# Performance work log

Measured on AMD Instinct MI355X. Metric: run time of the kernel, lower is better.

The kernel has to match this reference:

```python
import jax, jax.numpy as jnp
import numpy as np

B, S, HID = 1, 1024, 4096
H, D = 32, 128
KB, NUM_SLOTS, KB_IDX = 2048, 2, 0
TOPK = 100
THETA = 10000.0
KB_SCALE = 100.0
NEG = -1e9


def _rope(x, pos):
    # x: [B,H,S,D], pos: [B,S]
    inv = 1.0 / (THETA ** (jnp.arange(0, D, 2, dtype=jnp.float32) / D))
    freqs = pos[..., None].astype(jnp.float32) * inv          # [B,S,D/2]
    emb = jnp.concatenate([freqs, freqs], -1)                  # [B,S,D]
    cos = jnp.cos(emb)[:, None]                                # [B,1,S,D]
    sin = jnp.sin(emb)[:, None]
    x1, x2 = jnp.split(x, 2, -1)
    rot = jnp.concatenate([-x2, x1], -1)
    return x * cos + rot * sin


def setup_inputs() -> dict:
    key = jax.random.key(0)
    ks = jax.random.split(key, 8)
    hidden_states = jax.random.normal(ks[0], (B, S, HID), jnp.float32)
    # standard additive causal mask (0 on allowed, large negative above diagonal)
    causal = jnp.tril(jnp.ones((S, S), bool))
    attention_mask = jnp.where(causal, 0.0, NEG).astype(jnp.float32)[None, None]
    position_ids = jnp.arange(S, dtype=jnp.int64 if jax.config.jax_enable_x64 else jnp.int32)[None].astype(jnp.int32)
    kb_keys = jax.random.normal(ks[1], (KB, NUM_SLOTS * HID), jnp.float32)
    kb_values = jax.random.normal(ks[2], (KB, NUM_SLOTS * HID), jnp.float32)
    std = 0.02
    Wq = jax.random.normal(ks[3], (HID, HID), jnp.float32) * std
    Wq2 = jax.random.normal(ks[4], (HID, HID), jnp.float32) * std
    Wk = jax.random.normal(ks[5], (HID, HID), jnp.float32) * std
    Wv = jax.random.normal(ks[6], (HID, HID), jnp.float32) * std
    Wo = jax.random.normal(ks[7], (HID, HID), jnp.float32) * std
    score_shift = jnp.zeros((H, 1), jnp.float32) - 3.0
    return dict(hidden_states=hidden_states, attention_mask=attention_mask,
                position_ids=position_ids, kb_keys=kb_keys, kb_values=kb_values,
                Wq=Wq, Wq2=Wq2, Wk=Wk, Wv=Wv, Wo=Wo, score_shift=score_shift)


def reference(hidden_states, attention_mask, position_ids, kb_keys, kb_values,
              Wq, Wq2, Wk, Wv, Wo, score_shift):
    b, s, _ = hidden_states.shape
    heads = lambda x: x.reshape(b, s, H, D).transpose(0, 2, 1, 3)
    q = heads(hidden_states @ Wq.T)
    q2 = heads(hidden_states @ Wq2.T)
    k = heads(hidden_states @ Wk.T)
    v = heads(hidden_states @ Wv.T)
    q = _rope(q, position_ids)
    k = _rope(k, position_ids)
    scale = 1.0 / jnp.sqrt(jnp.asarray(D, jnp.float32))

    # ---- KB branch (2-dim kb_kvs, layer_idx % kb_layer_frequency == 0) ----
    kbk = kb_keys.reshape(KB, NUM_SLOTS, HID)[:, KB_IDX].reshape(KB, H, D).transpose(1, 0, 2)  # [H,KB,D]
    kbv = kb_values.reshape(KB, NUM_SLOTS, HID)[:, KB_IDX].reshape(KB, H, D).transpose(1, 0, 2)
    kbk = jnp.broadcast_to(kbk[None], (b, H, KB, D))
    kbv = jnp.broadcast_to(kbv[None], (b, H, KB, D))

    # dynamic_sparsify: top-k pruning of KB entries by summed q2-scores
    aw2_full = jnp.einsum('bhqd,bhkd->bhqk', q2, kbk) * scale     # [b,H,S,KB]
    kb_scores = jax.lax.stop_gradient(aw2_full.sum((1, 2)))       # [b,KB]
    _, top_idx = jax.lax.top_k(kb_scores, TOPK)                   # [b,TOPK]
    gather = jax.vmap(lambda a, i: a[:, i])                        # [H,KB,D],[TOPK]->[H,TOPK,D]
    kbk_t = gather(kbk, top_idx)
    kbv_t = gather(kbv, top_idx)

    keys = jnp.concatenate([kbk_t, k], 2)                         # [b,H,TOPK+S,D]
    vals = jnp.concatenate([kbv_t, v], 2)

    aw = jnp.einsum('bhqd,bhkd->bhqk', q, keys) * scale           # [b,H,S,TOPK+S]

    # sep_query_head: KB logits use q2, per-head score_shift, log scale-factor correction
    aw2 = jnp.einsum('bhqd,bhkd->bhqk', q2, kbk_t) * scale        # [b,H,S,TOPK]
    aw2 = aw2 + score_shift.reshape(1, H, 1, 1)
    aw2 = aw2 - jnp.log(jnp.asarray(TOPK, jnp.float32)) + jnp.log(jnp.asarray(KB_SCALE, jnp.float32))
    aw = jnp.concatenate([aw2, aw[..., TOPK:]], -1)

    # mask: KB columns fully visible (no fully-padded rows in causal mask)
    kb_mask = jnp.zeros((b, 1, s, TOPK), attention_mask.dtype)
    mask = jnp.concatenate([kb_mask, attention_mask], -1)
    probs = jax.nn.softmax((aw + mask).astype(jnp.float32), -1).astype(q.dtype)

    out = jnp.einsum('bhqk,bhkd->bhqd', probs, vals)
    out = out.transpose(0, 2, 1, 3).reshape(b, s, HID)
    return out @ Wo.T
```

## Files before the change

### kernel.cpp

```cpp
#include <hip/hip_runtime.h>
#include <hip/hip_bf16.h>
#include <math.h>

typedef __hip_bfloat16 bf16_t;
typedef __attribute__((ext_vector_type(8))) short short8;
typedef __attribute__((ext_vector_type(4))) float f32x4;

#define S_LEN 1024
#define HID   4096
#define NH    32
#define HD    128
#define KB_N  2048
#define TOPK  100
#define SCALE 0.08838834764831845f

typedef const __attribute__((address_space(1))) void* gptr_t;
typedef __attribute__((address_space(3))) void* lptr_t;

__global__ void k0_zero(float* __restrict__ out, float* __restrict__ hssum) {
  int tid = threadIdx.x;
  if (blockIdx.x < 4096) {
    float4 z = {0.f, 0.f, 0.f, 0.f};
    *(float4*)(out + ((size_t)blockIdx.x * 256 + tid) * 4) = z;
  } else {
    float4 z = {0.f, 0.f, 0.f, 0.f};
    *(float4*)(hssum + tid * 4) = z;
    *(float4*)(hssum + 1024 + tid * 4) = z;
    *(float4*)(hssum + 2048 + tid * 4) = z;
    *(float4*)(hssum + 3072 + tid * 4) = z;
  }
}

__global__ void kw_conv(const float* __restrict__ Wq, const float* __restrict__ Wq2,
                        const float* __restrict__ Wk, const float* __restrict__ Wv,
                        const float* __restrict__ Wo,
                        bf16_t* __restrict__ Wcat, bf16_t* __restrict__ Wob) {
  int w = blockIdx.y;
  const float* src = (w == 0) ? Wq : (w == 1) ? Wq2 : (w == 2) ? Wk : (w == 3) ? Wv : Wo;
  bf16_t* dst = (w < 4) ? (Wcat + (size_t)w * 16777216) : Wob;
  size_t i = ((size_t)blockIdx.x * 256 + threadIdx.x) * 4;
  float4 f = *(const float4*)(src + i);
  union { bf16_t h[4]; uint2 u; } p;
  p.h[0] = __float2bfloat16(f.x); p.h[1] = __float2bfloat16(f.y);
  p.h[2] = __float2bfloat16(f.z); p.h[3] = __float2bfloat16(f.w);
  *(uint2*)(dst + i) = p.u;
}

__global__ void k1_convert(const float* __restrict__ hs, bf16_t* __restrict__ hsb) {
  size_t i = ((size_t)blockIdx.x * 256 + threadIdx.x) * 4;
  float4 f = *(const float4*)(hs + i);
  union { bf16_t h[4]; uint2 u; } p;
  p.h[0] = __float2bfloat16(f.x); p.h[1] = __float2bfloat16(f.y);
  p.h[2] = __float2bfloat16(f.z); p.h[3] = __float2bfloat16(f.w);
  *(uint2*)(hsb + i) = p.u;
}

__global__ void k1_colsum(const float* __restrict__ hs, float* __restrict__ hssum) {
  int col = blockIdx.x * 256 + threadIdx.x;
  int r0 = blockIdx.y * 64;
  float acc = 0.f;
#pragma unroll 8
  for (int r = 0; r < 64; r++) acc += hs[(size_t)(r0 + r) * HID + col];
  atomicAdd(hssum + col, acc);
}

__global__ void k2_q2sum(const float* __restrict__ W,
                         const float* __restrict__ hssum,
                         float* __restrict__ q2sum) {
  int wave = threadIdx.x >> 6, lane = threadIdx.x & 63;
  int row = blockIdx.x * 4 + wave;
  const float4* wr = (const float4*)(W + (size_t)row * HID);
  const float4* xr = (const float4*)hssum;
  float acc = 0.f;
#pragma unroll
  for (int it = 0; it < 16; it++) {
    float4 a = wr[it * 64 + lane];
    float4 b = xr[it * 64 + lane];
    acc += a.x * b.x + a.y * b.y + a.z * b.z + a.w * b.w;
  }
#pragma unroll
  for (int off = 32; off > 0; off >>= 1) acc += __shfl_xor(acc, off, 64);
  if (lane == 0) q2sum[row] = acc;
}

__global__ void k3_kbscore(const float* __restrict__ kbk,
                           const float* __restrict__ q2sum,
                           float* __restrict__ scores) {
  int wave = threadIdx.x >> 6, lane = threadIdx.x & 63;
  int row = blockIdx.x * 4 + wave;
  const float4* kr = (const float4*)(kbk + (size_t)row * 8192);
  const float4* xr = (const float4*)q2sum;
  float acc = 0.f;
#pragma unroll
  for (int it = 0; it < 16; it++) {
    float4 a = kr[it * 64 + lane];
    float4 b = xr[it * 64 + lane];
    acc += a.x * b.x + a.y * b.y + a.z * b.z + a.w * b.w;
  }
#pragma unroll
  for (int off = 32; off > 0; off >>= 1) acc += __shfl_xor(acc, off, 64);
  if (lane == 0) scores[row] = acc * SCALE;
}

__global__ void k4_topk(const float* __restrict__ scores, int* __restrict__ tidx) {
  int lane = threadIdx.x;
  float v[32];
#pragma unroll
  for (int i = 0; i < 32; i++) v[i] = scores[i * 64 + lane];
  for (int t = 0; t < TOPK; t++) {
    float bm = -INFINITY; int bi = 0x7fffffff;
#pragma unroll
    for (int i = 0; i < 32; i++) {
      if (v[i] > bm) { bm = v[i]; bi = i * 64 + lane; }
    }
#pragma unroll
    for (int off = 32; off > 0; off >>= 1) {
      float ov = __shfl_xor(bm, off, 64);
      int   oi = __shfl_xor(bi, off, 64);
      if (ov > bm || (ov == bm && oi < bi)) { bm = ov; bi = oi; }
    }
    if (lane == 0) tidx[t] = bi;
    if ((bi & 63) == lane) {
      int slot = bi >> 6;
#pragma unroll
      for (int i = 0; i < 32; i++) if (i == slot) v[i] = -INFINITY;
    }
  }
}

__global__ void k5_gather(const float* __restrict__ kbk, const float* __restrict__ kbv,
                          const int* __restrict__ tidx,
                          bf16_t* __restrict__ kbkt, bf16_t* __restrict__ kbvt) {
  int j = blockIdx.x;
  int tid = threadIdx.x;
  if (j < TOPK) {
    size_t src = (size_t)tidx[j] * 8192;
#pragma unroll
    for (int r = 0; r < 4; r++) {
      int i = (tid + r * 256) * 4;
      float4 a = *(const float4*)(kbk + src + i);
      float4 b = *(const float4*)(kbv + src + i);
      union { bf16_t h[4]; uint2 u; } pa, pb;
      pa.h[0] = __float2bfloat16(a.x); pa.h[1] = __float2bfloat16(a.y);
      pa.h[2] = __float2bfloat16(a.z); pa.h[3] = __float2bfloat16(a.w);
      pb.h[0] = __float2bfloat16(b.x); pb.h[1] = __float2bfloat16(b.y);
      pb.h[2] = __float2bfloat16(b.z); pb.h[3] = __float2bfloat16(b.w);
      *(uint2*)(kbkt + (size_t)j * HID + i) = pa.u;
      *(uint2*)(kbvt + (size_t)j * HID + i) = pb.u;
    }
  } else {
    uint2 z; z.x = 0u; z.y = 0u;
#pragma unroll
    for (int r = 0; r < 4; r++) {
      int i = (tid + r * 256) * 4;
      *(uint2*)(kbkt + (size_t)j * HID + i) = z;
      *(uint2*)(kbvt + (size_t)j * HID + i) = z;
    }
  }
}

template<int MODE>
__global__ __launch_bounds__(256) void gemm_dma(
    const bf16_t* __restrict__ A, const bf16_t* __restrict__ B,
    void* O0, void* O1, void* O2, void* O3) {
  __shared__ bf16_t As[128 * 32];
  __shared__ bf16_t Bs[128 * 32];
  const int tid = threadIdx.x;
  const int wave = tid >> 6, lane = tid & 63;
  const int bm = blockIdx.y * 128;
  const int bn = blockIdx.x * 128;
  const int lrow = lane & 15, quad = lane >> 4;
  const int wr = wave >> 1, wc = wave & 1;
  const int srow = lane >> 2, sch = lane & 3;

  f32x4 acc[4][4];
  const f32x4 zero4 = {0.f, 0.f, 0.f, 0.f};
#pragma unroll
  for (int i = 0; i < 4; i++)
#pragma unroll
    for (int j = 0; j < 4; j++) acc[i][j] = zero4;

  const int kbeg = (MODE == 1) ? blockIdx.z * 1024 : 0;
  const int kend = (MODE == 1) ? kbeg + 1024 : 4096;

  for (int k0 = kbeg; k0 < kend; k0 += 32) {
    __syncthreads();
#pragma unroll
    for (int h = 0; h < 2; h++) {
      int rg = wave * 32 + h * 16;
      __builtin_amdgcn_global_load_lds(
          (gptr_t)(A + (size_t)(bm + rg + srow) * 4096 + k0 + sch * 8),
          (lptr_t)(As + rg * 32), 16, 0, 0);
      __builtin_amdgcn_global_load_lds(
          (gptr_t)(B + (size_t)(bn + rg + srow) * 4096 + k0 + sch * 8),
          (lptr_t)(Bs + rg * 32), 16, 0, 0);
    }
    __syncthreads();
    short8 af[4], bfr[4];
#pragma unroll
    for (int i = 0; i < 4; i++)
      af[i] = *(const short8*)(As + (wr * 64 + i * 16 + lrow) * 32 + quad * 8);
#pragma unroll
    for (int j = 0; j < 4; j++)
      bfr[j] = *(const short8*)(Bs + (wc * 64 + j * 16 + lrow) * 32 + quad * 8);
#pragma unroll
    for (int i = 0; i < 4; i++)
#pragma unroll
      for (int j = 0; j < 4; j++)
        acc[i][j] = __builtin_amdgcn_mfma_f32_16x16x32_bf16(af[i], bfr[j], acc[i][j], 0, 0, 0);
  }

  if (MODE == 0) {
    bf16_t* dst = (bf16_t*)((bn >> 12) == 0 ? O0 : (bn >> 12) == 1 ? O1
                          : (bn >> 12) == 2 ? O2 : O3);
    int nb = bn & 4095;
#pragma unroll
    for (int i = 0; i < 4; i++)
#pragma unroll
      for (int j = 0; j < 4; j++)
#pragma unroll
        for (int r = 0; r < 4; r++) {
          int m = bm + wr * 64 + i * 16 + quad * 4 + r;
          int n = nb + wc * 64 + j * 16 + lrow;
          dst[(size_t)m * 4096 + n] = __float2bfloat16(acc[i][j][r]);
        }
  } else {
    float* dst = (float*)O0;
#pragma unroll
    for (int i = 0; i < 4; i++)
#pragma unroll
      for (int j = 0; j < 4; j++)
#pragma unroll
        for (int r = 0; r < 4; r++) {
          int m = bm + wr * 64 + i * 16 + quad * 4 + r;
          int n = bn + wc * 64 + j * 16 + lrow;
          atomicAdd(dst + (size_t)m * 4096 + n, acc[i][j][r]);
        }
  }
}

template<int OUT_BF16>
__global__ __launch_bounds__(256) void gemm_bt(
    const bf16_t* __restrict__ A,
    const float* __restrict__ B0, const float* __restrict__ B1,
    const float* __restrict__ B2, const float* __restrict__ B3,
    void* C0, void* C1, void* C2, void* C3) {
  const int z = blockIdx.z;
  const float* __restrict__ B = (z == 0) ? B0 : (z == 1) ? B1 : (z == 2) ? B2 : B3;
  void* Cv = (z == 0) ? C0 : (z == 1) ? C1 : (z == 2) ? C2 : C3;
  __shared__ bf16_t As[128][40];
  __shared__ bf16_t Bs[128][40];
  const int tid = threadIdx.x;
  const int bm = blockIdx.y * 128, bn = blockIdx.x * 128;
  const int wave = tid >> 6, lane = tid & 63;
  const int wr = wave >> 1, wc = wave & 1;
  const int lrow = lane & 15, quad = lane >> 4;
  f32x4 acc[4][4];
  const f32x4 zero4 = {0.f, 0.f, 0.f, 0.f};
#pragma unroll
  for (int i = 0; i < 4; i++)
#pragma unroll
    for (int j = 0; j < 4; j++) acc[i][j] = zero4;
  const int arow = tid >> 2, ach = tid & 3;
  const int brow = tid >> 3, bch = tid & 7;
  for (int k0 = 0; k0 < 4096; k0 += 32) {
    __syncthreads();
#pragma unroll
    for (int r = 0; r < 2; r++) {
      int row = arow + r * 64;
      uint4 val = *(const uint4*)(A + (size_t)(bm + row) * 4096 + k0 + ach * 8);
      *(uint4*)(&As[row][ach * 8]) = val;
    }
#pragma unroll
    for (int r = 0; r < 4; r++) {
      int row = brow + r * 32;
      float4 f = *(const float4*)(B + (size_t)(bn + row) * 4096 + k0 + bch * 4);
      union { bf16_t h[4]; uint2 u; } p;
      p.h[0] = __float2bfloat16(f.x); p.h[1] = __float2bfloat16(f.y);
      p.h[2] = __float2bfloat16(f.z); p.h[3] = __float2bfloat16(f.w);
      *(uint2*)(&Bs[row][bch * 4]) = p.u;
    }
    __syncthreads();
    short8 af[4], bfr[4];
#pragma unroll
    for (int i = 0; i < 4; i++)
      af[i] = *(const short8*)(&As[wr * 64 + i * 16 + lrow][quad * 8]);
#pragma unroll
    for (int j = 0; j < 4; j++)
      bfr[j] = *(const short8*)(&Bs[wc * 64 + j * 16 + lrow][quad * 8]);
#pragma unroll
    for (int i = 0; i < 4; i++)
#pragma unroll
      for (int j = 0; j < 4; j++)
        acc[i][j] = __builtin_amdgcn_mfma_f32_16x16x32_bf16(af[i], bfr[j], acc[i][j], 0, 0, 0);
  }
#pragma unroll
  for (int i = 0; i < 4; i++)
#pragma unroll
    for (int j = 0; j < 4; j++)
#pragma unroll
      for (int r = 0; r < 4; r++) {
        int m = bm + wr * 64 + i * 16 + quad * 4 + r;
        int n = bn + wc * 64 + j * 16 + lrow;
        if (OUT_BF16)
          ((bf16_t*)Cv)[(size_t)m * 4096 + n] = __float2bfloat16(acc[i][j][r]);
        else
          ((float*)Cv)[(size_t)m * 4096 + n] = acc[i][j][r];
      }
}

__global__ void k7_rope(bf16_t* __restrict__ q, bf16_t* __restrict__ k,
                        const int* __restrict__ pos_ids) {
  int t = blockIdx.x * 256 + threadIdx.x;
  int d = t & 63;
  int h = (t >> 6) & 31;
  int s = t >> 11;
  float pos = (float)pos_ids[s];
  float inv = exp2f(-(float)d * 0.20762050593046f);
  float ang = pos * inv;
  float c = cosf(ang), si = sinf(ang);
  size_t i1 = (size_t)s * HID + h * HD + d;
  size_t i2 = i1 + 64;
  float a1 = __bfloat162float(q[i1]), a2 = __bfloat162float(q[i2]);
  q[i1] = __float2bfloat16(a1 * c - a2 * si);
  q[i2] = __float2bfloat16(a2 * c + a1 * si);
  float b1 = __bfloat162float(k[i1]), b2 = __bfloat162float(k[i2]);
  k[i1] = __float2bfloat16(b1 * c - b2 * si);
  k[i2] = __float2bfloat16(b2 * c + b1 * si);
}

#define FA_PAD 136
__global__ __launch_bounds__(256) void k8_flash(
    const bf16_t* __restrict__ qg, const bf16_t* __restrict__ q2g,
    const bf16_t* __restrict__ kg, const bf16_t* __restrict__ vg,
    const bf16_t* __restrict__ kbkt, const bf16_t* __restrict__ kbvt,
    const float* __restrict__ shift_p,
    bf16_t* __restrict__ outb) {
  __shared__ bf16_t KV[128][FA_PAD];
  __shared__ bf16_t Ps[4][16][FA_PAD];
  int qt = 15 - (int)blockIdx.x;
  int h = blockIdx.y;
  int q0 = qt * 64;
  int tid = threadIdx.x;
  int wave = tid >> 6, lane = tid & 63;
  int lrow = lane & 15, quad = lane >> 4;

  short8 qf[4], q2f[4];
  {
    const size_t base = (size_t)(q0 + wave * 16 + lrow) * HID + h * HD;
#pragma unroll
    for (int kc = 0; kc < 4; kc++) {
      qf[kc]  = *(const short8*)(qg  + base + kc * 32 + quad * 8);
      q2f[kc] = *(const short8*)(q2g + base + kc * 32 + quad * 8);
    }
  }
  const f32x4 zero4 = {0.f, 0.f, 0.f, 0.f};
  f32x4 O[8];
#pragma unroll
  for (int df = 0; df < 8; df++) O[df] = zero4;
  float m_i[4], l_i[4];
#pragma unroll
  for (int r = 0; r < 4; r++) { m_i[r] = -INFINITY; l_i[r] = 0.f; }
  float shift = shift_p[h];

  int nt = (q0 + 63) / 128 + 1;
  for (int tile = -1; tile < nt; tile++) {
    const bf16_t* ksrc = (tile < 0) ? (kbkt + h * HD)
                                    : (kg + (size_t)tile * 128 * HID + h * HD);
    const bf16_t* vsrc = (tile < 0) ? (kbvt + h * HD)
                                    : (vg + (size_t)tile * 128 * HID + h * HD);
    __syncthreads();
    {
      int rbase = tid >> 4, ch = tid & 15;
#pragma unroll
      for (int rr = 0; rr < 8; rr++) {
        int row = rr * 16 + rbase;
        uint4 val = *(const uint4*)(ksrc + (size_t)row * HID + ch * 8);
        *(uint4*)(&KV[row][ch * 8]) = val;
      }
    }
    __syncthreads();
    f32x4 Sv[8];
#pragma unroll
    for (int jf = 0; jf < 8; jf++) {
      short8 kf[4];
#pragma unroll
      for (int kc = 0; kc < 4; kc++)
        kf[kc] = *(const short8*)(&KV[jf * 16 + lrow][kc * 32 + quad * 8]);
      f32x4 s = zero4;
      if (tile < 0) {
#pragma unroll
        for (int kc = 0; kc < 4; kc++)
          s = __builtin_amdgcn_mfma_f32_16x16x32_bf16(q2f[kc], kf[kc], s, 0, 0, 0);
      } else {
#pragma unroll
        for (int kc = 0; kc < 4; kc++)
          s = __builtin_amdgcn_mfma_f32_16x16x32_bf16(qf[kc], kf[kc], s, 0, 0, 0);
      }
      Sv[jf] = s;
    }
#pragma unroll
    for (int jf = 0; jf < 8; jf++)
#pragma unroll
      for (int r = 0; r < 4; r++) {
        float val = Sv[jf][r] * SCALE;
        if (tile < 0) {
          val += shift;
          int col = jf * 16 + lrow;
          if (col >= TOPK) val = -1e30f;
        } else {
          int srow = q0 + wave * 16 + quad * 4 + r;
          int tcol = tile * 128 + jf * 16 + lrow;
          if (tcol > srow) val -= 1e9f;
        }
        Sv[jf][r] = val;
      }
    float alpha[4];
#pragma unroll
    for (int r = 0; r < 4; r++) {
      float tm = Sv[0][r];
#pragma unroll
      for (int jf = 1; jf < 8; jf++) tm = fmaxf(tm, Sv[jf][r]);
#pragma unroll
      for (int off = 1; off < 16; off <<= 1) tm = fmaxf(tm, __shfl_xor(tm, off, 64));
      float mn = fmaxf(m_i[r], tm);
      alpha[r] = __expf(m_i[r] - mn);
      m_i[r] = mn;
    }
    float rsum[4] = {0.f, 0.f, 0.f, 0.f};
#pragma unroll
    for (int jf = 0; jf < 8; jf++)
#pragma unroll
      for (int r = 0; r < 4; r++) {
        float p = __expf(Sv[jf][r] - m_i[r]);
        Sv[jf][r] = p;
        rsum[r] += p;
      }
#pragma unroll
    for (int r = 0; r < 4; r++) {
#pragma unroll
      for (int off = 1; off < 16; off <<= 1) rsum[r] += __shfl_xor(rsum[r], off, 64);
      l_i[r] = l_i[r] * alpha[r] + rsum[r];
    }
#pragma unroll
    for (int jf = 0; jf < 8; jf++)
#pragma unroll
      for (int r = 0; r < 4; r++)
        Ps[wave][quad * 4 + r][jf * 16 + lrow] = __float2bfloat16(Sv[jf][r]);
#pragma unroll
    for (int df = 0; df < 8; df++)
#pragma unroll
      for (int r = 0; r < 4; r++) O[df][r] *= alpha[r];
    __syncthreads();
    {
      int rbase = tid >> 4, ch = tid & 15;
#pragma unroll
      for (int rr = 0; rr < 8; rr++) {
        int t = rr * 16 + rbase;
        union { uint4 u; bf16_t hx[8]; } vv;
        vv.u = *(const uint4*)(vsrc + (size_t)t * HID + ch * 8);
        int cs = ((t >> 3) ^ ch) & 15;
        int tl = t & 7;
#pragma unroll
        for (int e = 0; e < 8; e++)
          KV[ch * 8 + e][cs * 8 + tl] = vv.hx[e];
      }
    }
    __syncthreads();
    short8 pf[4];
#pragma unroll
    for (int kc = 0; kc < 4; kc++)
      pf[kc] = *(const short8*)(&Ps[wave][lrow][kc * 32 + quad * 8]);
#pragma unroll
    for (int df = 0; df < 8; df++) {
      int d = df * 16 + lrow;
      int sw = (d >> 3) & 15;
#pragma unroll
      for (int kc = 0; kc < 4; kc++) {
        short8 vf = *(const short8*)(&KV[d][(((kc * 4 + quad) ^ sw) & 15) * 8]);
        O[df] = __builtin_amdgcn_mfma_f32_16x16x32_bf16(pf[kc], vf, O[df], 0, 0, 0);
      }
    }
  }
#pragma unroll
  for (int df = 0; df < 8; df++)
#pragma unroll
    for (int r = 0; r < 4; r++) {
      int srow = q0 + wave * 16 + quad * 4 + r;
      float val = O[df][r] / l_i[r];
      outb[(size_t)srow * HID + h * HD + df * 16 + lrow] = __float2bfloat16(val);
    }
}

extern "C" void kernel_launch(void* const* d_in, const int* in_sizes, int n_in,
                              void* d_out, int out_size, void* d_ws, size_t ws_size,
                              hipStream_t stream) {
  const float* hs    = (const float*)d_in[0];
  const int*   pos   = (const int*)d_in[2];
  const float* kbk   = (const float*)d_in[3];
  const float* kbv   = (const float*)d_in[4];
  const float* Wq    = (const float*)d_in[5];
  const float* Wq2   = (const float*)d_in[6];
  const float* Wk    = (const float*)d_in[7];
  const float* Wv    = (const float*)d_in[8];
  const float* Wo    = (const float*)d_in[9];
  const float* shift = (const float*)d_in[10];
  float* out = (float*)d_out;

  char* ws = (char*)d_ws;
  const size_t MB8 = 8388608;
  bf16_t* qb    = (bf16_t*)(ws);
  bf16_t* q2b   = (bf16_t*)(ws + MB8);
  bf16_t* kbuf  = (bf16_t*)(ws + 2 * MB8);
  bf16_t* vbuf  = (bf16_t*)(ws + 3 * MB8);
  bf16_t* hsb   = (bf16_t*)(ws + 4 * MB8);
  bf16_t* kbkt  = (bf16_t*)(ws + 5 * MB8);
  bf16_t* kbvt  = (bf16_t*)(ws + 5 * MB8 + 1048576);
  float*  hssum = (float*)(ws + 5 * MB8 + 2 * 1048576);
  float*  q2s   = (float*)(ws + 5 * MB8 + 2 * 1048576 + 16384);
  float*  scr   = (float*)(ws + 5 * MB8 + 2 * 1048576 + 32768);
  int*    tidx  = (int*)(ws + 5 * MB8 + 2 * 1048576 + 40960);
  bf16_t* attnb = hsb;
  const size_t WCAT_OFF = 48ull * 1048576;
  bf16_t* Wcat = (bf16_t*)(ws + WCAT_OFF);
  bf16_t* Wob  = (bf16_t*)(ws + WCAT_OFF + 134217728);
  const size_t WS_NEED = WCAT_OFF + 134217728 + 33554432;
  const bool big_ws = (ws_size >= WS_NEED);

  k0_zero<<<dim3(4097), dim3(256), 0, stream>>>(out, hssum);
  if (big_ws)
    kw_conv<<<dim3(16384, 5), dim3(256), 0, stream>>>(Wq, Wq2, Wk, Wv, Wo, Wcat, Wob);
  k1_convert<<<dim3(4096), dim3(256), 0, stream>>>(hs, hsb);
  k1_colsum<<<dim3(16, 16), dim3(256), 0, stream>>>(hs, hssum);
  k2_q2sum<<<dim3(1024), dim3(256), 0, stream>>>(Wq2, hssum, q2s);
  k3_kbscore<<<dim3(512), dim3(256), 0, stream>>>(kbk, q2s, scr);
  k4_topk<<<dim3(1), dim3(64), 0, stream>>>(scr, tidx);
  k5_gather<<<dim3(128), dim3(256), 0, stream>>>(kbk, kbv, tidx, kbkt, kbvt);

  if (big_ws) {
    gemm_dma<0><<<dim3(128, 8), dim3(256), 0, stream>>>(
        hsb, Wcat, (void*)qb, (void*)q2b, (void*)kbuf, (void*)vbuf);
  } else {
    gemm_bt<1><<<dim3(32, 8, 4), dim3(256), 0, stream>>>(
        hsb, Wq, Wq2, Wk, Wv, (void*)qb, (void*)q2b, (void*)kbuf, (void*)vbuf);
  }
  k7_rope<<<dim3(8192), dim3(256), 0, stream>>>(qb, kbuf, pos);
  k8_flash<<<dim3(16, 32), dim3(256), 0, stream>>>(
      qb, q2b, kbuf, vbuf, kbkt, kbvt, shift, attnb);
  if (big_ws) {
    gemm_dma<1><<<dim3(32, 8, 4), dim3(256), 0, stream>>>(
        attnb, Wob, (void*)out, nullptr, nullptr, nullptr);
  } else {
    gemm_bt<0><<<dim3(32, 8, 1), dim3(256), 0, stream>>>(
        attnb, Wo, Wo, Wo, Wo, (void*)out, (void*)out, (void*)out, (void*)out);
  }
}
```

Measured before the change: 909.2 us.

## Replace 128x128 DMA GEMM with 256x256 four-stage pipelined swizzled GEMM

The projection and output GEMMs move from 128x128 tiles with 256 threads and two barriers per k-step to 256x256 tiles with 512 threads. Global-to-LDS loads run through a 4-deep ring buffer, using explicit vmcnt waits and a single barrier per step, so loads overlap the MFMA work. An XOR swizzle on LDS chunks is meant to cut bank conflicts, and s_setprio is raised around the MFMA bursts. Each block now needs 128KB of LDS and more accumulator registers, and the grids become 256 blocks, which limits occupancy to one block per CU.

```diff
diff --git a/kernel.cpp b/kernel.cpp
--- a/kernel.cpp
+++ b/kernel.cpp
@@ -16,6 +16,10 @@
 
 typedef const __attribute__((address_space(1))) void* gptr_t;
 typedef __attribute__((address_space(3))) void* lptr_t;
+
+#define VM8 asm volatile("s_waitcnt vmcnt(8)" ::: "memory")
+#define VM4 asm volatile("s_waitcnt vmcnt(4)" ::: "memory")
+#define VM0 asm volatile("s_waitcnt vmcnt(0)" ::: "memory")
 
 __global__ void k0_zero(float* __restrict__ out, float* __restrict__ hssum) {
   int tid = threadIdx.x;
@@ -160,79 +164,107 @@
 }
 
 template<int MODE>
-__global__ __launch_bounds__(256) void gemm_dma(
+__global__ __launch_bounds__(512, 2) void gemm_256(
     const bf16_t* __restrict__ A, const bf16_t* __restrict__ B,
     void* O0, void* O1, void* O2, void* O3) {
-  __shared__ bf16_t As[128 * 32];
-  __shared__ bf16_t Bs[128 * 32];
-  const int tid = threadIdx.x;
+  __shared__ __attribute__((aligned(16))) bf16_t sm[4 * 16384];
+  const int tid  = threadIdx.x;
   const int wave = tid >> 6, lane = tid & 63;
-  const int bm = blockIdx.y * 128;
-  const int bn = blockIdx.x * 128;
   const int lrow = lane & 15, quad = lane >> 4;
-  const int wr = wave >> 1, wc = wave & 1;
-  const int srow = lane >> 2, sch = lane & 3;
-
-  f32x4 acc[4][4];
+  const int wr = wave >> 2, wc = wave & 3;
+  const int bm = blockIdx.y * 256;
+  const int bn = blockIdx.x * 256;
+  const int srow = tid >> 2;
+  const int lc   = (tid & 3) ^ ((srow >> 1) & 3);
+  const int pc   = quad ^ ((lrow >> 1) & 3);
+
+  const int kbeg = (MODE == 1) ? blockIdx.z * 1024 : 0;
+  const int NT   = (MODE == 1) ? 32 : 128;
+
+  const bf16_t* aS = A + (size_t)(bm + srow) * 4096 + kbeg + lc * 8;
+  const bf16_t* bS = B + (size_t)(bn + srow) * 4096 + kbeg + lc * 8;
+  bf16_t* const lw = sm + wave * 512;
+
+  f32x4 acc[8][4];
   const f32x4 zero4 = {0.f, 0.f, 0.f, 0.f};
 #pragma unroll
-  for (int i = 0; i < 4; i++)
+  for (int i = 0; i < 8; i++)
 #pragma unroll
     for (int j = 0; j < 4; j++) acc[i][j] = zero4;
 
-  const int kbeg = (MODE == 1) ? blockIdx.z * 1024 : 0;
-  const int kend = (MODE == 1) ? kbeg + 1024 : 4096;
-
-  for (int k0 = kbeg; k0 < kend; k0 += 32) {
-    __syncthreads();
-#pragma unroll
-    for (int h = 0; h < 2; h++) {
-      int rg = wave * 32 + h * 16;
-      __builtin_amdgcn_global_load_lds(
-          (gptr_t)(A + (size_t)(bm + rg + srow) * 4096 + k0 + sch * 8),
-          (lptr_t)(As + rg * 32), 16, 0, 0);
-      __builtin_amdgcn_global_load_lds(
-          (gptr_t)(B + (size_t)(bn + rg + srow) * 4096 + k0 + sch * 8),
-          (lptr_t)(Bs + rg * 32), 16, 0, 0);
-    }
-    __syncthreads();
+  auto STAGE = [&](int tt) {
+    bf16_t* l = lw + (tt & 3) * 16384;
+    const bf16_t* ga = aS + tt * 32;
+    const bf16_t* gb = bS + tt * 32;
+    __builtin_amdgcn_global_load_lds((gptr_t)ga,             (lptr_t)l,           16, 0, 0);
+    __builtin_amdgcn_global_load_lds((gptr_t)(ga + 524288),  (lptr_t)(l + 4096),  16, 0, 0);
+    __builtin_amdgcn_global_load_lds((gptr_t)gb,             (lptr_t)(l + 8192),  16, 0, 0);
+    __builtin_amdgcn_global_load_lds((gptr_t)(gb + 524288),  (lptr_t)(l + 12288), 16, 0, 0);
+  };
+
+  STAGE(0); STAGE(1); STAGE(2);
+  VM8;
+  __builtin_amdgcn_s_barrier();
+
+  auto body = [&](int t, bool do_stage) {
+    const bf16_t* Ab = sm + (t & 3) * 16384 + (wr * 128 + lrow) * 32 + pc * 8;
+    const bf16_t* Bb = sm + (t & 3) * 16384 + 8192 + (wc * 64 + lrow) * 32 + pc * 8;
+    if (do_stage) STAGE(t + 3);
     short8 af[4], bfr[4];
 #pragma unroll
-    for (int i = 0; i < 4; i++)
-      af[i] = *(const short8*)(As + (wr * 64 + i * 16 + lrow) * 32 + quad * 8);
-#pragma unroll
-    for (int j = 0; j < 4; j++)
-      bfr[j] = *(const short8*)(Bs + (wc * 64 + j * 16 + lrow) * 32 + quad * 8);
+    for (int j = 0; j < 4; j++) bfr[j] = *(const short8*)(Bb + j * 512);
+#pragma unroll
+    for (int i = 0; i < 4; i++) af[i] = *(const short8*)(Ab + i * 512);
+    __builtin_amdgcn_s_setprio(1);
 #pragma unroll
     for (int i = 0; i < 4; i++)
 #pragma unroll
       for (int j = 0; j < 4; j++)
         acc[i][j] = __builtin_amdgcn_mfma_f32_16x16x32_bf16(af[i], bfr[j], acc[i][j], 0, 0, 0);
-  }
+    __builtin_amdgcn_s_setprio(0);
+#pragma unroll
+    for (int i = 0; i < 4; i++) af[i] = *(const short8*)(Ab + (i + 4) * 512);
+    __builtin_amdgcn_s_setprio(1);
+#pragma unroll
+    for (int i = 0; i < 4; i++)
+#pragma unroll
+      for (int j = 0; j < 4; j++)
+        acc[i + 4][j] = __builtin_amdgcn_mfma_f32_16x16x32_bf16(af[i], bfr[j], acc[i + 4][j], 0, 0, 0);
+    __builtin_amdgcn_s_setprio(0);
+  };
+
+  for (int t = 0; t < NT - 3; ++t) {
+    body(t, true);
+    VM8;
+    __builtin_amdgcn_s_barrier();
+  }
+  body(NT - 3, false); VM4; __builtin_amdgcn_s_barrier();
+  body(NT - 2, false); VM0; __builtin_amdgcn_s_barrier();
+  body(NT - 1, false);
 
   if (MODE == 0) {
     bf16_t* dst = (bf16_t*)((bn >> 12) == 0 ? O0 : (bn >> 12) == 1 ? O1
                           : (bn >> 12) == 2 ? O2 : O3);
-    int nb = bn & 4095;
-#pragma unroll
-    for (int i = 0; i < 4; i++)
+    const int nb = bn & 4095;
+#pragma unroll
+    for (int i = 0; i < 8; i++)
 #pragma unroll
       for (int j = 0; j < 4; j++)
 #pragma unroll
         for (int r = 0; r < 4; r++) {
-          int m = bm + wr * 64 + i * 16 + quad * 4 + r;
+          int m = bm + wr * 128 + i * 16 + quad * 4 + r;
           int n = nb + wc * 64 + j * 16 + lrow;
           dst[(size_t)m * 4096 + n] = __float2bfloat16(acc[i][j][r]);
         }
   } else {
     float* dst = (float*)O0;
 #pragma unroll
-    for (int i = 0; i < 4; i++)
+    for (int i = 0; i < 8; i++)
 #pragma unroll
       for (int j = 0; j < 4; j++)
 #pragma unroll
         for (int r = 0; r < 4; r++) {
-          int m = bm + wr * 64 + i * 16 + quad * 4 + r;
+          int m = bm + wr * 128 + i * 16 + quad * 4 + r;
           int n = bn + wc * 64 + j * 16 + lrow;
           atomicAdd(dst + (size_t)m * 4096 + n, acc[i][j][r]);
         }
@@ -538,7 +570,7 @@
   k5_gather<<<dim3(128), dim3(256), 0, stream>>>(kbk, kbv, tidx, kbkt, kbvt);
 
   if (big_ws) {
-    gemm_dma<0><<<dim3(128, 8), dim3(256), 0, stream>>>(
+    gemm_256<0><<<dim3(64, 4), dim3(512), 0, stream>>>(
         hsb, Wcat, (void*)qb, (void*)q2b, (void*)kbuf, (void*)vbuf);
   } else {
     gemm_bt<1><<<dim3(32, 8, 4), dim3(256), 0, stream>>>(
@@ -548,7 +580,7 @@
   k8_flash<<<dim3(16, 32), dim3(256), 0, stream>>>(
       qb, q2b, kbuf, vbuf, kbkt, kbvt, shift, attnb);
   if (big_ws) {
-    gemm_dma<1><<<dim3(32, 8, 4), dim3(256), 0, stream>>>(
+    gemm_256<1><<<dim3(16, 4, 4), dim3(512), 0, stream>>>(
         attnb, Wob, (void*)out, nullptr, nullptr, nullptr);
   } else {
     gemm_bt<0><<<dim3(32, 8, 1), dim3(256), 0, stream>>>(
```

New measurement: 809.8 us. 1.12x faster.
